# Kernel optimization log

Hardware: AMD Instinct MI355X
Metric: run time of the kernel (lower is better)

Reference implementation:

```python
import jax, jax.numpy as jnp
import numpy as np

WS = (7, 7, 7)          # window size (S, H, W)
NUM_HEADS = 6
DIM = 192
B_, NW = 128, 32        # total windows, windows per image (mask dim)
N = WS[0] * WS[1] * WS[2]  # 343 tokens per window


def _relative_position_index():
    # Faithful replica of the torch __init__ logic (incl. indexing='xy' and
    # the 3*W1-1 / 2*W1-1 multipliers).
    cs = np.arange(WS[0]); ch = np.arange(WS[1]); cw = np.arange(WS[2])
    coords = np.stack(np.meshgrid(cs, ch, cw, indexing='xy'))  # (3, Wh, Ws, Ww)
    cf = coords.reshape(3, -1)                                  # (3, N)
    rel = cf[:, :, None] - cf[:, None, :]                       # (3, N, N)
    rel = rel.transpose(1, 2, 0).astype(np.int64)               # (N, N, 3)
    rel[:, :, 0] += WS[0] - 1
    rel[:, :, 1] += WS[1] - 1
    rel[:, :, 2] += WS[2] - 1
    rel[:, :, 0] *= 3 * WS[1] - 1
    rel[:, :, 1] *= 2 * WS[1] - 1
    return rel.sum(-1)                                          # (N, N) int


def setup_inputs() -> dict:
    key = jax.random.key(0)
    ks = jax.random.split(key, 6)
    C = DIM
    x = jax.random.normal(ks[0], (B_, N, C), dtype=jnp.float32)
    mask = jax.random.normal(ks[1], (NW, N, N), dtype=jnp.float32)
    qkv_w = jax.random.normal(ks[2], (3 * C, C), dtype=jnp.float32) * 0.02
    qkv_b = jnp.zeros((3 * C,), dtype=jnp.float32)
    proj_w = jax.random.normal(ks[3], (C, C), dtype=jnp.float32) * 0.02
    proj_b = jnp.zeros((C,), dtype=jnp.float32)
    table_len = (2 * WS[0] - 1) * (2 * WS[1] - 1) * (2 * WS[2] - 1)
    rpb_table = jax.random.normal(ks[4], (table_len, NUM_HEADS), dtype=jnp.float32) * 0.02
    rel_index = jnp.asarray(_relative_position_index(), dtype=jnp.int32)
    return {"x": x, "mask": mask, "qkv_w": qkv_w, "qkv_b": qkv_b,
            "proj_w": proj_w, "proj_b": proj_b, "rpb_table": rpb_table,
            "rel_index": rel_index}


def reference(x, mask, qkv_w, qkv_b, proj_w, proj_b, rpb_table, rel_index):
    B, n, C = x.shape
    H = NUM_HEADS
    hd = C // H
    scale = hd ** (-0.5)
    qkv = x @ qkv_w.T + qkv_b                      # (B, N, 3C)
    qkv = qkv.reshape(B, n, 3, H, hd).transpose(2, 0, 3, 1, 4)  # (3, B, H, N, hd)
    q, k, v = qkv[0] * scale, qkv[1], qkv[2]
    attn = jnp.einsum('bhnd,bhmd->bhnm', q, k)     # (B, H, N, N)
    bias = rpb_table[rel_index.reshape(-1)].reshape(n, n, H)
    attn = attn + bias.transpose(2, 0, 1)[None]    # (B, H, N, N)
    nW = mask.shape[0]
    attn = attn.reshape(B // nW, nW, H, n, n) + mask[None, :, None]
    attn = jax.nn.softmax(attn.reshape(B, H, n, n), axis=-1)
    out = jnp.einsum('bhnm,bhmd->bhnd', attn, v)   # (B, H, N, hd)
    out = out.transpose(0, 2, 1, 3).reshape(B, n, C)
    return out @ proj_w.T + proj_b
```

## Files before the change

kernel.cpp:

```cpp
#include <hip/hip_runtime.h>
#include <hip/hip_fp16.h>
#include <hip/hip_bf16.h>
#include <stdint.h>

#define WN 343
#define NH 6
#define HD 32
#define CD 192
#define NB 128
#define NWM 32
#define BMROW 352
#define BMSLICE (11*16*BMROW)
#define BMKC (16*BMROW)
#define LOG2E 1.4426950408889634f

typedef __attribute__((ext_vector_type(8))) short short8;
typedef __attribute__((ext_vector_type(4))) float f32x4;

__device__ __forceinline__ unsigned short f2bf(float f) {
  union { float f; uint32_t u; } v; v.f = f;
  uint32_t r = v.u + 0x7fffu + ((v.u >> 16) & 1u);
  return (unsigned short)(r >> 16);
}

__device__ __forceinline__ uint32_t pk2bf(float a, float b) {
  __hip_bfloat162 h = __float22bfloat162_rn(make_float2(a, b));
  return *(uint32_t*)&h;
}

__device__ __forceinline__ uint32_t pkh2(float a, float b) {
  __half2 h; h.x = __float2half(a); h.y = __float2half(b);
  return *(uint32_t*)&h;
}

typedef const __attribute__((address_space(1))) unsigned int* gas_ptr;
typedef __attribute__((address_space(3))) unsigned int* las_ptr;
__device__ __forceinline__ void gload16(const unsigned short* g, unsigned short* l) {
  __builtin_amdgcn_global_load_lds((gas_ptr)(const void*)g, (las_ptr)(void*)l, 16, 0, 0);
}

__global__ __launch_bounds__(256) void prep_bm_kernel(
    const int* __restrict__ rel, const float* __restrict__ rpb,
    const float* __restrict__ mask, uint32_t* __restrict__ bP,
    uint32_t* __restrict__ mP) {
  __shared__ float M[352][33];
  const int bid = blockIdx.x;
  const int tid = threadIdx.x;
  if (bid < 264) {
    const int h = bid / 44;
    const int rem = bid - h * 44;
    const int kc = rem >> 2;
    const int g = rem & 3;
    const int n0 = g * 88;
    const int k0 = kc * 32;
    for (int idx = tid; idx < 88 * 32; idx += 256) {
      int nl = idx >> 5, k = idx & 31;
      int n = n0 + nl;
      int nc = (n < WN) ? n : (WN - 1);
      M[nl][k] = (k0 + k < WN) ? rpb[rel[nc * WN + k0 + k] * NH + h] * LOG2E
                               : -30000.0f;
    }
    __syncthreads();
    uint32_t* outp = bP + (size_t)h * BMSLICE + (size_t)kc * BMKC;
    if (tid < 88) {
      const int nl = tid;
      const int n = n0 + nl;
#pragma unroll
      for (int quad = 0; quad < 4; ++quad) {
        uint4 o;
        o.x = pkh2(M[nl][quad * 8 + 0], M[nl][quad * 8 + 4]);
        o.y = pkh2(M[nl][quad * 8 + 1], M[nl][quad * 8 + 5]);
        o.z = pkh2(M[nl][quad * 8 + 2], M[nl][quad * 8 + 6]);
        o.w = pkh2(M[nl][quad * 8 + 3], M[nl][quad * 8 + 7]);
        *(uint4*)(outp + ((size_t)quad * 352 + n) * 4) = o;
      }
    }
    return;
  }
  const int sub = bid - 264;
  const int wdx = sub / 11;
  const int kc = sub - wdx * 11;
  const int k0 = kc * 32;
  const float* mw = mask + (size_t)wdx * (WN * WN);
  for (int idx = tid; idx < 352 * 32; idx += 256) {
    int n = idx >> 5, k = idx & 31;
    M[n][k] = (n < WN && k0 + k < WN) ? mw[n * WN + k0 + k] * LOG2E : 0.0f;
  }
  __syncthreads();
  uint32_t* outp = mP + (size_t)wdx * BMSLICE + (size_t)kc * BMKC;
#pragma unroll
  for (int quad = 0; quad < 4; ++quad) {
#pragma unroll
    for (int j = 0; j < 2; ++j) {
      int n = tid + 256 * j;
      if (n < 352) {
        uint4 o;
        o.x = pkh2(M[n][quad * 8 + 0], M[n][quad * 8 + 4]);
        o.y = pkh2(M[n][quad * 8 + 1], M[n][quad * 8 + 5]);
        o.z = pkh2(M[n][quad * 8 + 2], M[n][quad * 8 + 6]);
        o.w = pkh2(M[n][quad * 8 + 3], M[n][quad * 8 + 7]);
        *(uint4*)(outp + ((size_t)quad * 352 + n) * 4) = o;
      }
    }
  }
}

__global__ __launch_bounds__(256) void prep_cvt_kernel(
    const float* __restrict__ wq, const float* __restrict__ wp,
    const float* __restrict__ x, unsigned short* __restrict__ wqb,
    unsigned short* __restrict__ wpb, unsigned short* __restrict__ xb) {
  const int tid = threadIdx.x;
  int cb = blockIdx.x;
  if (cb < 54) {
    int g = cb * 256 + tid;
    int sk = g / 768; int rem = g - sk * 768;
    int row = rem >> 2; int cc = rem & 3;
    int s = sk / 6; int kt = sk - s * 6;
    int lch = cc ^ ((row >> 1) & 3);
    const float* src = wq + (size_t)(s * 192 + row) * CD + kt * 32 + lch * 8;
    f32x4 a = *(const f32x4*)src;
    f32x4 b = *(const f32x4*)(src + 4);
    union { short8 v8; uint32_t d[4]; } pk;
    pk.d[0] = pk2bf(a[0], a[1]);
    pk.d[1] = pk2bf(a[2], a[3]);
    pk.d[2] = pk2bf(b[0], b[1]);
    pk.d[3] = pk2bf(b[2], b[3]);
    *(short8*)(wqb + (size_t)g * 8) = pk.v8;
    return;
  }
  cb -= 54;
  if (cb < 18) {
    int g = cb * 256 + tid;
    int kt = g / 768; int rem = g - kt * 768;
    int row = rem >> 2; int cc = rem & 3;
    int lch = cc ^ ((row >> 1) & 3);
    const float* src = wp + (size_t)row * CD + kt * 32 + lch * 8;
    f32x4 a = *(const f32x4*)src;
    f32x4 b = *(const f32x4*)(src + 4);
    union { short8 v8; uint32_t d[4]; } pk;
    pk.d[0] = pk2bf(a[0], a[1]);
    pk.d[1] = pk2bf(a[2], a[3]);
    pk.d[2] = pk2bf(b[0], b[1]);
    pk.d[3] = pk2bf(b[2], b[3]);
    *(short8*)(wpb + (size_t)g * 8) = pk.v8;
    return;
  }
  cb -= 18;
  size_t gx = (size_t)cb * 256 + tid;
  int tile = (int)(gx >> 9); int rem = (int)(gx & 511);
  int row = rem >> 2; int cc = rem & 3;
  int mb = tile / 6; int kt = tile - mb * 6;
  int lch = cc ^ ((row >> 1) & 3);
  const float* src = x + ((size_t)mb * 128 + row) * CD + kt * 32 + lch * 8;
  f32x4 a = *(const f32x4*)src;
  f32x4 b = *(const f32x4*)(src + 4);
  union { short8 v8; uint32_t d[4]; } pk;
  pk.d[0] = pk2bf(a[0], a[1]);
  pk.d[1] = pk2bf(a[2], a[3]);
  pk.d[2] = pk2bf(b[0], b[1]);
  pk.d[3] = pk2bf(b[2], b[3]);
  *(short8*)(xb + gx * 8) = pk.v8;
}

__global__ __launch_bounds__(256) void qkv_kernel(
    const unsigned short* __restrict__ xb, const unsigned short* __restrict__ wqb,
    const float* __restrict__ bvec,
    unsigned short* __restrict__ qb, unsigned short* __restrict__ kb,
    unsigned short* __restrict__ vb) {
  __shared__ __align__(16) unsigned short SL[10240];
  unsigned short* XL = SL;
  unsigned short* WL = SL + 4096;
  const int tid = threadIdx.x;
  const int wave = tid >> 6, lane = tid & 63;
  const int quad = lane >> 4, c = lane & 15;
  const int m0 = blockIdx.x * 128;
  const int s = blockIdx.y;
  const int chk = (quad ^ ((c >> 1) & 3)) * 8;

  f32x4 acc[2][12];
#pragma unroll
  for (int i = 0; i < 2; ++i)
#pragma unroll
    for (int j = 0; j < 12; ++j) acc[i][j] = (f32x4){0.f, 0.f, 0.f, 0.f};

  const size_t xt0 = (size_t)blockIdx.x * 6;
  const size_t wt0 = (size_t)s * 6;
  for (int kt = 0; kt < 6; ++kt) {
    const unsigned short* gx = xb + ((xt0 + kt) << 12) + tid * 8;
    const unsigned short* gw = wqb + (wt0 + kt) * 6144 + tid * 8;
    unsigned short* lx = XL + (size_t)wave * 512;
    unsigned short* lw = WL + (size_t)wave * 512;
    gload16(gx, lx);
    gload16(gx + 2048, lx + 2048);
    gload16(gw, lw);
    gload16(gw + 2048, lw + 2048);
    gload16(gw + 4096, lw + 4096);
    __syncthreads();
    short8 af0 = *(const short8*)&XL[(wave * 32 + c) * 32 + chk];
    short8 af1 = *(const short8*)&XL[(wave * 32 + 16 + c) * 32 + chk];
#pragma unroll
    for (int j = 0; j < 12; ++j) {
      short8 bfr = *(const short8*)&WL[(j * 16 + c) * 32 + chk];
      acc[0][j] = __builtin_amdgcn_mfma_f32_16x16x32_bf16(af0, bfr, acc[0][j], 0, 0, 0);
      acc[1][j] = __builtin_amdgcn_mfma_f32_16x16x32_bf16(af1, bfr, acc[1][j], 0, 0, 0);
    }
    __syncthreads();
  }

  const float qscale = 0.25503486f;
  unsigned short* dst = (s == 0) ? qb : ((s == 1) ? kb : vb);
  const float scl = (s == 0) ? qscale : 1.0f;
  const int n0 = s * 192;
  unsigned short* Lh0 = SL;
  unsigned short* Lh1 = SL + 4608;
  for (int hh = 0; hh < 3; ++hh) {
    __syncthreads();
#pragma unroll
    for (int jj = 0; jj < 4; ++jj) {
      int j = hh * 4 + jj;
      int hl = jj >> 1;
      int dd = (jj & 1) * 16 + c;
      float bn = bvec[n0 + j * 16 + c];
      unsigned short* L = hl ? Lh1 : Lh0;
#pragma unroll
      for (int i = 0; i < 2; ++i)
#pragma unroll
        for (int r = 0; r < 4; ++r) {
          int m = wave * 32 + i * 16 + quad * 4 + r;
          L[m * 36 + dd] = f2bf((acc[i][j][r] + bn) * scl);
        }
    }
    __syncthreads();
    const int m = tid & 127;
    const int hl = tid >> 7;
    const int M = m0 + m;
    const int b = M / WN;
    const int tok = M - b * WN;
    const int h = hh * 2 + hl;
    const unsigned short* L = hl ? Lh1 : Lh0;
    unsigned short* drow = dst + (((size_t)b * NH + h) * WN + tok) * HD;
#pragma unroll
    for (int t2 = 0; t2 < 4; ++t2) {
      int d0 = t2 * 8;
      *(short8*)&drow[d0] = *(const short8*)&L[m * 36 + d0];
    }
  }
}

__global__ __launch_bounds__(512) void attn_kernel(
    const unsigned short* __restrict__ qb, const unsigned short* __restrict__ kb,
    const unsigned short* __restrict__ vb, const uint32_t* __restrict__ biasP,
    const uint32_t* __restrict__ maskP, unsigned short* __restrict__ ob) {
  __shared__ __align__(16) unsigned short Ks[352][40];
  __shared__ __align__(16) unsigned short Vt[HD][360];
  const int bid = blockIdx.x;
  const int job = (bid & 7) * 96 + (bid >> 3);
  const int wdx = job / 24;
  const int inner = job - wdx * 24;
  const int h = inner >> 2;
  const int b = (inner & 3) * 32 + wdx;
  const int tid = threadIdx.x;
  const int wave = tid >> 6, lane = tid & 63;
  const int quad = lane >> 4, c = lane & 15;
  const size_t base = ((size_t)b * NH + h) * (WN * HD);
  const unsigned short* q = qb + base;
  const unsigned short* k = kb + base;
  const unsigned short* v = vb + base;
  const uint32_t* bS = biasP + (size_t)h * BMSLICE;
  const uint32_t* mS = maskP + (size_t)wdx * BMSLICE;

  for (int t = tid; t < WN * 4; t += 512) {
    int r = t >> 2, ch = t & 3;
    int kk = r & 31;
    int row = (r & ~31) + 16 * ((kk >> 2) & 1) + 4 * (kk >> 3) + (kk & 3);
    *(short8*)&Ks[row][ch * 8] = *(const short8*)(k + r * HD + ch * 8);
  }
  for (int t = tid; t < 9 * 32; t += 512) {
    int kg = WN + (t >> 5);
    int kk = kg & 31;
    int row = (kg & ~31) + 16 * ((kk >> 2) & 1) + 4 * (kk >> 3) + (kk & 3);
    Ks[row][t & 31] = 0;
  }
  for (int t = tid; t < WN; t += 512) {
#pragma unroll
    for (int ch = 0; ch < 4; ++ch) {
      short8 vv = *(const short8*)(v + t * HD + ch * 8);
#pragma unroll
      for (int j = 0; j < 8; ++j) Vt[ch * 8 + j][t] = vv[j];
    }
  }
  for (int t = tid; t < 9 * 32; t += 512) {
    Vt[t & 31][WN + (t >> 5)] = 0;
  }
  __syncthreads();

  for (int qt = wave; qt < 22; qt += 8) {
    const int q0 = qt * 16;
    int qr = q0 + c; if (qr > WN - 1) qr = WN - 1;
    const short8 qf = *(const short8*)(q + qr * HD + quad * 8);
    const uint32_t* bRow = bS + ((size_t)quad * 352 + q0 + c) * 4;
    const uint32_t* mRow = mS + ((size_t)quad * 352 + q0 + c) * 4;

    f32x4 o0 = (f32x4){0.f, 0.f, 0.f, 0.f}, o1 = (f32x4){0.f, 0.f, 0.f, 0.f};
    float l = 0.f;
#pragma unroll 2
    for (int kc = 0; kc < 11; ++kc) {
      uint4 bw4 = *(const uint4*)(bRow + (size_t)kc * BMKC);
      uint4 mw4 = *(const uint4*)(mRow + (size_t)kc * BMKC);
      f32x4 cc0, cc1;
      {
        __half2 s2; float2 f;
        s2 = __hadd2(*(__half2*)&bw4.x, *(__half2*)&mw4.x);
        f = __half22float2(s2); cc0[0] = f.x; cc1[0] = f.y;
        s2 = __hadd2(*(__half2*)&bw4.y, *(__half2*)&mw4.y);
        f = __half22float2(s2); cc0[1] = f.x; cc1[1] = f.y;
        s2 = __hadd2(*(__half2*)&bw4.z, *(__half2*)&mw4.z);
        f = __half22float2(s2); cc0[2] = f.x; cc1[2] = f.y;
        s2 = __hadd2(*(__half2*)&bw4.w, *(__half2*)&mw4.w);
        f = __half22float2(s2); cc0[3] = f.x; cc1[3] = f.y;
      }
      const int k0 = kc * 32;
      short8 kf0 = *(const short8*)&Ks[k0 + c][quad * 8];
      short8 kf1 = *(const short8*)&Ks[k0 + 16 + c][quad * 8];
      f32x4 s0 = __builtin_amdgcn_mfma_f32_16x16x32_bf16(kf0, qf, cc0, 0, 0, 0);
      f32x4 s1 = __builtin_amdgcn_mfma_f32_16x16x32_bf16(kf1, qf, cc1, 0, 0, 0);
      float p0 = __builtin_amdgcn_exp2f(s0[0]), p1 = __builtin_amdgcn_exp2f(s0[1]);
      float p2 = __builtin_amdgcn_exp2f(s0[2]), p3 = __builtin_amdgcn_exp2f(s0[3]);
      float p4 = __builtin_amdgcn_exp2f(s1[0]), p5 = __builtin_amdgcn_exp2f(s1[1]);
      float p6 = __builtin_amdgcn_exp2f(s1[2]), p7 = __builtin_amdgcn_exp2f(s1[3]);
      l += (p0 + p1 + p2 + p3) + (p4 + p5 + p6 + p7);
      union { short8 v8; uint32_t d[4]; } pf;
      pf.d[0] = pk2bf(p0, p1);
      pf.d[1] = pk2bf(p2, p3);
      pf.d[2] = pk2bf(p4, p5);
      pf.d[3] = pk2bf(p6, p7);
      short8 vf0 = *(const short8*)&Vt[c][k0 + quad * 8];
      short8 vf1 = *(const short8*)&Vt[16 + c][k0 + quad * 8];
      o0 = __builtin_amdgcn_mfma_f32_16x16x32_bf16(pf.v8, vf0, o0, 0, 0, 0);
      o1 = __builtin_amdgcn_mfma_f32_16x16x32_bf16(pf.v8, vf1, o1, 0, 0, 0);
    }
    l += __shfl_xor(l, 16);
    l += __shfl_xor(l, 32);

#pragma unroll
    for (int r = 0; r < 4; ++r) {
      int n = q0 + quad * 4 + r;
      if (n < WN) {
        float lq = __shfl(l, quad * 4 + r, 16);
        float inv = 1.0f / lq;
        int M = b * WN + n;
        int rloc = M & 127;
        int xr = (rloc >> 1) & 3;
        size_t base2 = (((size_t)(M >> 7) * 6 + h) << 12) + rloc * 32;
        ob[base2 + (((c >> 3) ^ xr) << 3) + (c & 7)] = f2bf(o0[r] * inv);
        ob[base2 + ((((c >> 3) | 2) ^ xr) << 3) + (c & 7)] = f2bf(o1[r] * inv);
      }
    }
  }
}

__global__ __launch_bounds__(256) void proj_kernel(
    const unsigned short* __restrict__ obp, const unsigned short* __restrict__ wpb,
    const float* __restrict__ bvec, float* __restrict__ out) {
  __shared__ __align__(16) unsigned short SL[8192];
  unsigned short* XL = SL;
  unsigned short* WL = SL + 2048;
  const int tid = threadIdx.x;
  const int wave = tid >> 6, lane = tid & 63;
  const int quad = lane >> 4, c = lane & 15;
  const int m0 = blockIdx.x * 64;
  const int mb = blockIdx.x >> 1;
  const int r0 = (blockIdx.x & 1) * 64;
  const int chk = (quad ^ ((c >> 1) & 3)) * 8;

  f32x4 acc[12];
#pragma unroll
  for (int j = 0; j < 12; ++j) acc[j] = (f32x4){0.f, 0.f, 0.f, 0.f};

  for (int kt = 0; kt < 6; ++kt) {
    const unsigned short* gx =
        obp + (((size_t)mb * 6 + kt) << 12) + r0 * 32 + tid * 8;
    const unsigned short* gw = wpb + (size_t)kt * 6144 + tid * 8;
    unsigned short* lx = XL + (size_t)wave * 512;
    unsigned short* lw = WL + (size_t)wave * 512;
    gload16(gx, lx);
    gload16(gw, lw);
    gload16(gw + 2048, lw + 2048);
    gload16(gw + 4096, lw + 4096);
    __syncthreads();
    short8 af = *(const short8*)&XL[(wave * 16 + c) * 32 + chk];
#pragma unroll
    for (int j = 0; j < 12; ++j) {
      short8 bfr = *(const short8*)&WL[(j * 16 + c) * 32 + chk];
      acc[j] = __builtin_amdgcn_mfma_f32_16x16x32_bf16(af, bfr, acc[j], 0, 0, 0);
    }
    __syncthreads();
  }

#pragma unroll
  for (int j = 0; j < 12; ++j) {
    int col = j * 16 + c;
    float bn = bvec[col];
#pragma unroll
    for (int r = 0; r < 4; ++r) {
      int m = m0 + wave * 16 + quad * 4 + r;
      out[(size_t)m * CD + col] = acc[j][r] + bn;
    }
  }
}

extern "C" void kernel_launch(void* const* d_in, const int* in_sizes, int n_in,
                              void* d_out, int out_size, void* d_ws, size_t ws_size,
                              hipStream_t stream) {
  const float* x      = (const float*)d_in[0];
  const float* mask   = (const float*)d_in[1];
  const float* qkv_w  = (const float*)d_in[2];
  const float* qkv_b  = (const float*)d_in[3];
  const float* proj_w = (const float*)d_in[4];
  const float* proj_b = (const float*)d_in[5];
  const float* rpb    = (const float*)d_in[6];
  const int*   rel    = (const int*)d_in[7];
  float* out = (float*)d_out;

  char* ws = (char*)d_ws;
  uint32_t* biasP = (uint32_t*)ws;
  size_t off = 1486848;
  uint32_t* maskP = (uint32_t*)(ws + off); off += 7929856;
  unsigned short* qb = (unsigned short*)(ws + off); off += 16859136;
  unsigned short* kb = (unsigned short*)(ws + off); off += 16859136;
  unsigned short* vb = (unsigned short*)(ws + off); off += 16859136;
  unsigned short* wqb = (unsigned short*)(ws + off); off += 221184;
  unsigned short* wpb = (unsigned short*)(ws + off); off += 73728;
  unsigned short* xb  = (unsigned short*)(ws + off); off += 16859136;
  unsigned short* obuf = xb;

  hipLaunchKernelGGL(prep_cvt_kernel, dim3(54 + 18 + 4116), dim3(256), 0, stream,
                     qkv_w, proj_w, x, wqb, wpb, xb);
  hipLaunchKernelGGL(prep_bm_kernel, dim3(264 + 352), dim3(256), 0, stream,
                     rel, rpb, mask, biasP, maskP);
  hipLaunchKernelGGL(qkv_kernel, dim3(343, 3), dim3(256), 0, stream,
                     xb, wqb, qkv_b, qb, kb, vb);
  hipLaunchKernelGGL(attn_kernel, dim3(NH * NB), dim3(512), 0, stream,
                     qb, kb, vb, biasP, maskP, obuf);
  hipLaunchKernelGGL(proj_kernel, dim3(686), dim3(256), 0, stream,
                     obuf, wpb, proj_b, out);
}
```

Before: 219.6 us.

## Merge prep kernels, compute softmax row sums via MFMA, prefetch bias/mask

Merges the bias/mask prep and conversion kernels into one launch, and rewrites the mask prep to read directly from global memory without staging through LDS. In the attention loop, bias and mask for the next chunk are prefetched one iteration ahead. The scalar row-sum reduction and its shuffles are replaced by an extra MFMA against a ones vector, and MFMA blocks are wrapped in s_setprio. The MFMA row sum uses bf16-rounded probabilities, which slightly changes normalization numerics, and the unshared mask reads may be less coalesced.

New measurement: 215.8 us. About the same (-1.7%).

```diff
diff --git a/kernel.cpp b/kernel.cpp
--- a/kernel.cpp
+++ b/kernel.cpp
@@ -39,11 +39,14 @@
   __builtin_amdgcn_global_load_lds((gas_ptr)(const void*)g, (las_ptr)(void*)l, 16, 0, 0);
 }
 
-__global__ __launch_bounds__(256) void prep_bm_kernel(
+__global__ __launch_bounds__(256) void prep_kernel(
+    const float* __restrict__ wq, const float* __restrict__ wp,
+    unsigned short* __restrict__ wqb, unsigned short* __restrict__ wpb,
     const int* __restrict__ rel, const float* __restrict__ rpb,
     const float* __restrict__ mask, uint32_t* __restrict__ bP,
-    uint32_t* __restrict__ mP) {
-  __shared__ float M[352][33];
+    uint32_t* __restrict__ mP, const float* __restrict__ x,
+    unsigned short* __restrict__ xb) {
+  __shared__ float M[88][33];
   const int bid = blockIdx.x;
   const int tid = threadIdx.x;
   if (bid < 264) {
@@ -77,40 +80,38 @@
     }
     return;
   }
-  const int sub = bid - 264;
-  const int wdx = sub / 11;
-  const int kc = sub - wdx * 11;
-  const int k0 = kc * 32;
-  const float* mw = mask + (size_t)wdx * (WN * WN);
-  for (int idx = tid; idx < 352 * 32; idx += 256) {
-    int n = idx >> 5, k = idx & 31;
-    M[n][k] = (n < WN && k0 + k < WN) ? mw[n * WN + k0 + k] * LOG2E : 0.0f;
-  }
-  __syncthreads();
-  uint32_t* outp = mP + (size_t)wdx * BMSLICE + (size_t)kc * BMKC;
-#pragma unroll
-  for (int quad = 0; quad < 4; ++quad) {
-#pragma unroll
-    for (int j = 0; j < 2; ++j) {
-      int n = tid + 256 * j;
-      if (n < 352) {
-        uint4 o;
-        o.x = pkh2(M[n][quad * 8 + 0], M[n][quad * 8 + 4]);
-        o.y = pkh2(M[n][quad * 8 + 1], M[n][quad * 8 + 5]);
-        o.z = pkh2(M[n][quad * 8 + 2], M[n][quad * 8 + 6]);
-        o.w = pkh2(M[n][quad * 8 + 3], M[n][quad * 8 + 7]);
-        *(uint4*)(outp + ((size_t)quad * 352 + n) * 4) = o;
+  int cb = bid - 264;
+  if (cb < 352) {
+    const int wdx = cb / 11;
+    const int kc = cb - wdx * 11;
+    const int k0 = kc * 32;
+    const float* mw = mask + (size_t)wdx * (WN * WN);
+    uint32_t* outp = mP + (size_t)wdx * BMSLICE + (size_t)kc * BMKC;
+#pragma unroll
+    for (int quad = 0; quad < 4; ++quad) {
+      const int q8 = quad * 8;
+#pragma unroll
+      for (int j = 0; j < 2; ++j) {
+        int n = tid + 256 * j;
+        if (n < 352) {
+          float v[8];
+#pragma unroll
+          for (int i = 0; i < 8; ++i) {
+            int kk = k0 + q8 + i;
+            v[i] = (n < WN && kk < WN) ? mw[n * WN + kk] * LOG2E : 0.0f;
+          }
+          uint4 o;
+          o.x = pkh2(v[0], v[4]);
+          o.y = pkh2(v[1], v[5]);
+          o.z = pkh2(v[2], v[6]);
+          o.w = pkh2(v[3], v[7]);
+          *(uint4*)(outp + ((size_t)quad * 352 + n) * 4) = o;
+        }
       }
     }
-  }
-}
-
-__global__ __launch_bounds__(256) void prep_cvt_kernel(
-    const float* __restrict__ wq, const float* __restrict__ wp,
-    const float* __restrict__ x, unsigned short* __restrict__ wqb,
-    unsigned short* __restrict__ wpb, unsigned short* __restrict__ xb) {
-  const int tid = threadIdx.x;
-  int cb = blockIdx.x;
+    return;
+  }
+  cb -= 352;
   if (cb < 54) {
     int g = cb * 256 + tid;
     int sk = g / 768; int rem = g - sk * 768;
@@ -294,6 +295,9 @@
   }
   __syncthreads();
 
+  union { short8 v8; uint32_t d[4]; } on;
+  on.d[0] = on.d[1] = on.d[2] = on.d[3] = 0x3F803F80u;
+
   for (int qt = wave; qt < 22; qt += 8) {
     const int q0 = qt * 16;
     int qr = q0 + c; if (qr > WN - 1) qr = WN - 1;
@@ -301,34 +305,39 @@
     const uint32_t* bRow = bS + ((size_t)quad * 352 + q0 + c) * 4;
     const uint32_t* mRow = mS + ((size_t)quad * 352 + q0 + c) * 4;
 
-    f32x4 o0 = (f32x4){0.f, 0.f, 0.f, 0.f}, o1 = (f32x4){0.f, 0.f, 0.f, 0.f};
-    float l = 0.f;
-#pragma unroll 2
+    f32x4 o0 = (f32x4){0.f, 0.f, 0.f, 0.f};
+    f32x4 o1 = (f32x4){0.f, 0.f, 0.f, 0.f};
+    f32x4 accl = (f32x4){0.f, 0.f, 0.f, 0.f};
+    uint4 bw = *(const uint4*)bRow;
+    uint4 mw = *(const uint4*)mRow;
+#pragma unroll 1
     for (int kc = 0; kc < 11; ++kc) {
-      uint4 bw4 = *(const uint4*)(bRow + (size_t)kc * BMKC);
-      uint4 mw4 = *(const uint4*)(mRow + (size_t)kc * BMKC);
+      const int kcn = (kc < 10) ? kc + 1 : 10;
+      uint4 bwN = *(const uint4*)(bRow + (size_t)kcn * BMKC);
+      uint4 mwN = *(const uint4*)(mRow + (size_t)kcn * BMKC);
       f32x4 cc0, cc1;
       {
         __half2 s2; float2 f;
-        s2 = __hadd2(*(__half2*)&bw4.x, *(__half2*)&mw4.x);
+        s2 = __hadd2(*(__half2*)&bw.x, *(__half2*)&mw.x);
         f = __half22float2(s2); cc0[0] = f.x; cc1[0] = f.y;
-        s2 = __hadd2(*(__half2*)&bw4.y, *(__half2*)&mw4.y);
+        s2 = __hadd2(*(__half2*)&bw.y, *(__half2*)&mw.y);
         f = __half22float2(s2); cc0[1] = f.x; cc1[1] = f.y;
-        s2 = __hadd2(*(__half2*)&bw4.z, *(__half2*)&mw4.z);
+        s2 = __hadd2(*(__half2*)&bw.z, *(__half2*)&mw.z);
         f = __half22float2(s2); cc0[2] = f.x; cc1[2] = f.y;
-        s2 = __hadd2(*(__half2*)&bw4.w, *(__half2*)&mw4.w);
+        s2 = __hadd2(*(__half2*)&bw.w, *(__half2*)&mw.w);
         f = __half22float2(s2); cc0[3] = f.x; cc1[3] = f.y;
       }
       const int k0 = kc * 32;
       short8 kf0 = *(const short8*)&Ks[k0 + c][quad * 8];
       short8 kf1 = *(const short8*)&Ks[k0 + 16 + c][quad * 8];
+      __builtin_amdgcn_s_setprio(1);
       f32x4 s0 = __builtin_amdgcn_mfma_f32_16x16x32_bf16(kf0, qf, cc0, 0, 0, 0);
       f32x4 s1 = __builtin_amdgcn_mfma_f32_16x16x32_bf16(kf1, qf, cc1, 0, 0, 0);
+      __builtin_amdgcn_s_setprio(0);
       float p0 = __builtin_amdgcn_exp2f(s0[0]), p1 = __builtin_amdgcn_exp2f(s0[1]);
       float p2 = __builtin_amdgcn_exp2f(s0[2]), p3 = __builtin_amdgcn_exp2f(s0[3]);
       float p4 = __builtin_amdgcn_exp2f(s1[0]), p5 = __builtin_amdgcn_exp2f(s1[1]);
       float p6 = __builtin_amdgcn_exp2f(s1[2]), p7 = __builtin_amdgcn_exp2f(s1[3]);
-      l += (p0 + p1 + p2 + p3) + (p4 + p5 + p6 + p7);
       union { short8 v8; uint32_t d[4]; } pf;
       pf.d[0] = pk2bf(p0, p1);
       pf.d[1] = pk2bf(p2, p3);
@@ -336,18 +345,19 @@
       pf.d[3] = pk2bf(p6, p7);
       short8 vf0 = *(const short8*)&Vt[c][k0 + quad * 8];
       short8 vf1 = *(const short8*)&Vt[16 + c][k0 + quad * 8];
+      __builtin_amdgcn_s_setprio(1);
       o0 = __builtin_amdgcn_mfma_f32_16x16x32_bf16(pf.v8, vf0, o0, 0, 0, 0);
       o1 = __builtin_amdgcn_mfma_f32_16x16x32_bf16(pf.v8, vf1, o1, 0, 0, 0);
-    }
-    l += __shfl_xor(l, 16);
-    l += __shfl_xor(l, 32);
+      accl = __builtin_amdgcn_mfma_f32_16x16x32_bf16(pf.v8, on.v8, accl, 0, 0, 0);
+      __builtin_amdgcn_s_setprio(0);
+      bw = bwN; mw = mwN;
+    }
 
 #pragma unroll
     for (int r = 0; r < 4; ++r) {
       int n = q0 + quad * 4 + r;
       if (n < WN) {
-        float lq = __shfl(l, quad * 4 + r, 16);
-        float inv = 1.0f / lq;
+        float inv = 1.0f / accl[r];
         int M = b * WN + n;
         int rloc = M & 127;
         int xr = (rloc >> 1) & 3;
@@ -434,10 +444,9 @@
   unsigned short* xb  = (unsigned short*)(ws + off); off += 16859136;
   unsigned short* obuf = xb;
 
-  hipLaunchKernelGGL(prep_cvt_kernel, dim3(54 + 18 + 4116), dim3(256), 0, stream,
-                     qkv_w, proj_w, x, wqb, wpb, xb);
-  hipLaunchKernelGGL(prep_bm_kernel, dim3(264 + 352), dim3(256), 0, stream,
-                     rel, rpb, mask, biasP, maskP);
+  hipLaunchKernelGGL(prep_kernel, dim3(264 + 352 + 54 + 18 + 4116), dim3(256),
+                     0, stream,
+                     qkv_w, proj_w, wqb, wpb, rel, rpb, mask, biasP, maskP, x, xb);
   hipLaunchKernelGGL(qkv_kernel, dim3(343, 3), dim3(256), 0, stream,
                      xb, wqb, qkv_b, qb, kb, vb);
   hipLaunchKernelGGL(attn_kernel, dim3(NH * NB), dim3(512), 0, stream,
```
